# Kernel optimization log

Hardware: AMD Instinct MI355X
Metric: run time of the kernel (lower is better)

The kernel has to match this reference:

```python
import jax, jax.numpy as jnp
import numpy as np

EMB_DIM = 1024
ATT_DIM = 1024
N_HEADS = 16
HEAD_DIM = ATT_DIM // N_HEADS
ROPE_THETA = 10000.0


def setup_inputs() -> dict:
    key = jax.random.key(0)
    k1, k2, k3 = jax.random.split(key, 3)
    B, S = 2, 2048
    x = jax.random.normal(k1, (B, S, EMB_DIM), dtype=jnp.float32)
    # nn.Linear weights stored as [in, out] for x @ W
    W_qkv = jax.random.normal(k2, (EMB_DIM, 3 * ATT_DIM), dtype=jnp.float32) / np.sqrt(EMB_DIM)
    W_out = jax.random.normal(k3, (ATT_DIM, EMB_DIM), dtype=jnp.float32) / np.sqrt(ATT_DIM)
    return {"x": x, "W_qkv": W_qkv, "W_out": W_out}


def _rope_cos_sin(seq_len, dim, dtype):
    # rotary-embedding-torch: freqs over even indices, repeated interleaved
    inv_freq = 1.0 / (ROPE_THETA ** (jnp.arange(0, dim, 2, dtype=jnp.float32) / dim))
    t = jnp.arange(seq_len, dtype=jnp.float32)
    freqs = t[:, None] * inv_freq[None, :]            # [S, dim/2]
    freqs = jnp.repeat(freqs, 2, axis=-1)             # [S, dim] interleaved
    return jnp.cos(freqs).astype(dtype), jnp.sin(freqs).astype(dtype)


def _rotate_half(x):
    # interleaved pairs: (x0, x1) -> (-x1, x0)
    xr = x.reshape(x.shape[:-1] + (x.shape[-1] // 2, 2))
    x1, x2 = xr[..., 0], xr[..., 1]
    return jnp.stack([-x2, x1], axis=-1).reshape(x.shape)


def _apply_rope(x, cos, sin):
    # x: [B, H, S, D]; cos/sin: [S, D]
    return x * cos[None, None] + _rotate_half(x) * sin[None, None]


def reference(x, W_qkv, W_out):
    B, S, _ = x.shape
    qkv = x @ W_qkv                                   # [B, S, 3*ATT]
    qkv = qkv.reshape(B, S, 3, N_HEADS, HEAD_DIM)
    qkv = jnp.moveaxis(qkv, 3, 1)                     # [B, H, S, 3, D]
    q, k, v = qkv[..., 0, :], qkv[..., 1, :], qkv[..., 2, :]

    cos, sin = _rope_cos_sin(S, HEAD_DIM, x.dtype)
    q = _apply_rope(q, cos, sin)
    k = _apply_rope(k, cos, sin)

    scale = 1.0 / np.sqrt(HEAD_DIM)
    scores = jnp.einsum("bhqd,bhkd->bhqk", q, k) * scale
    attn = jax.nn.softmax(scores, axis=-1)
    out = jnp.einsum("bhqk,bhkd->bhqd", attn, v)      # [B, H, S, D]
    out = jnp.moveaxis(out, 1, 2).reshape(B, S, ATT_DIM)
    return out @ W_out                                # [B, S, EMB_DIM]
```

## Files before the change

kernel.cpp:

```cpp
#include <hip/hip_runtime.h>
#include <cstdint>
#include <cstddef>

typedef unsigned short u16;
typedef __bf16 bf16x8 __attribute__((ext_vector_type(8)));
typedef float f32x4 __attribute__((ext_vector_type(4)));

#define DEVI __device__ __forceinline__

constexpr int SEQ = 2048, NH = 16, HD = 64, EMB = 1024, N3 = 3072, MROWS = 4096;

DEVI u16 f2bf(float f) {
    union { float f; unsigned u; } x; x.f = f;
    unsigned r = (x.u + 0x7fffu + ((x.u >> 16) & 1u)) >> 16;
    return (u16)r;
}

DEVI f32x4 mfma16(bf16x8 a, bf16x8 b, f32x4 c) {
    return __builtin_amdgcn_mfma_f32_16x16x32_bf16(a, b, c, 0, 0, 0);
}

DEVI float exp2_raw(float x) {
    float r;
    asm("v_exp_f32 %0, %1" : "=v"(r) : "v"(x));
    return r;
}

#define GLDS16(g, l)                                                          \
    __builtin_amdgcn_global_load_lds(                                         \
        (__attribute__((address_space(1))) void*)(g),                         \
        (__attribute__((address_space(3))) void*)(l), 16, 0, 0)

__global__ __launch_bounds__(256) void prep_k(const float* __restrict__ x,
                                              const float* __restrict__ wqk,
                                              const float* __restrict__ wo,
                                              u16* __restrict__ xb, u16* __restrict__ wqkvT,
                                              u16* __restrict__ woutT, float2* __restrict__ tab) {
    __shared__ float tile[64][65];
    int bid = blockIdx.x, tid = threadIdx.x;
    if (bid < 4096) {
        int i = bid * 256 + tid;
        float4 v = ((const float4*)x)[i];
        ushort4 o;
        o.x = f2bf(v.x); o.y = f2bf(v.y); o.z = f2bf(v.z); o.w = f2bf(v.w);
        ((ushort4*)xb)[i] = o;
    } else if (bid < 5120) {
        const float* in; u16* out; int N, bx, by;
        if (bid < 4864) { in = wqk; out = wqkvT; N = 3072; int bb = bid - 4096; bx = bb % 48; by = bb / 48; }
        else            { in = wo;  out = woutT; N = 1024; int bb = bid - 4864; bx = bb % 16; by = bb / 16; }
        const int K = 1024;
        int k0 = by * 64, n0 = bx * 64;
        for (int i = 0; i < 16; i++) {
            int idx = i * 256 + tid;
            int r = idx >> 6, c = idx & 63;
            tile[r][c] = in[(size_t)(k0 + r) * N + n0 + c];
        }
        __syncthreads();
        for (int i = 0; i < 16; i++) {
            int idx = i * 256 + tid;
            int n = idx >> 6, k = idx & 63;
            out[(size_t)(n0 + n) * K + k0 + k] = f2bf(tile[k][n]);
        }
    } else {
        int idx = (bid - 5120) * 256 + tid;
        int t = idx >> 5, i = idx & 31;
        double ang = (double)t * pow(10000.0, -(double)i / 32.0);
        tab[idx] = make_float2((float)cos(ang), (float)sin(ang));
    }
}

template <int EPI>
__global__ __launch_bounds__(256) void gemm128_k(const u16* __restrict__ A, const u16* __restrict__ Bt,
                                                 int Kd, int Ncols,
                                                 u16* __restrict__ q_out, u16* __restrict__ k_out,
                                                 u16* __restrict__ v_out,
                                                 const float2* __restrict__ tab,
                                                 float* __restrict__ Cout) {
    __shared__ __align__(16) u16 smem[17408];
    u16* As = smem;
    u16* Bs = smem + 8192;
    int tid = threadIdx.x, lane = tid & 63, wv = tid >> 6;
    int wr = wv >> 1, wc = wv & 1;
    int l15 = lane & 15, lg = lane >> 4;
    int swr = l15 & 7;

    int nwg = gridDim.x * gridDim.y;
    int bid = blockIdx.y * gridDim.x + blockIdx.x;
    int swzb = (bid & 7) * (nwg >> 3) + (bid >> 3);
    int bx = swzb % gridDim.x, by = swzb / gridDim.x;
    int brow = by * 128, bcol = bx * 128;

    f32x4 acc[4][4];
    for (int i = 0; i < 4; i++)
        for (int j = 0; j < 4; j++) acc[i][j] = (f32x4){0.f, 0.f, 0.f, 0.f};

    const u16* Ab = A + (size_t)brow * Kd;
    const u16* Bb = Bt + (size_t)bcol * Kd;

    for (int kb = 0; kb < Kd; kb += 64) {
        for (int i = 0; i < 4; i++) {
            int cidx = i * 256 + tid;
            int rrow = cidx >> 3, c8 = cidx & 7;
            int sw = (c8 ^ (rrow & 7)) * 8;
            GLDS16(Ab + (size_t)rrow * Kd + kb + sw, As + cidx * 8);
            GLDS16(Bb + (size_t)rrow * Kd + kb + sw, Bs + cidx * 8);
        }
        __syncthreads();
#pragma unroll
        for (int kk = 0; kk < 2; kk++) {
            bf16x8 af[4], bf[4];
#pragma unroll
            for (int mi = 0; mi < 4; mi++)
                af[mi] = *(const bf16x8*)&As[(wr * 64 + mi * 16 + l15) * 64 +
                                             ((kk * 4 + lg) ^ swr) * 8];
#pragma unroll
            for (int ni = 0; ni < 4; ni++)
                bf[ni] = *(const bf16x8*)&Bs[(wc * 64 + ni * 16 + l15) * 64 +
                                             ((kk * 4 + lg) ^ swr) * 8];
#pragma unroll
            for (int mi = 0; mi < 4; mi++)
#pragma unroll
                for (int ni = 0; ni < 4; ni++)
                    acc[mi][ni] = mfma16(af[mi], bf[ni], acc[mi][ni]);
        }
        __syncthreads();
    }

    if constexpr (EPI == 0) {
        int c = bcol >> 10;
        int bb = brow >> 11, sbase = brow & 2047;
        int hbase = (bcol & 1023) >> 6;
        if (c == 2) {
            for (int mi = 0; mi < 4; mi++)
                for (int ni = 0; ni < 4; ni++) {
                    int col = wc * 64 + ni * 16 + l15;
                    int d = col & 63, h2 = col >> 6;
                    int s0 = sbase + wr * 64 + mi * 16 + lg * 4;
                    ushort4 pw;
                    pw.x = f2bf(acc[mi][ni][0]);
                    pw.y = f2bf(acc[mi][ni][1]);
                    pw.z = f2bf(acc[mi][ni][2]);
                    pw.w = f2bf(acc[mi][ni][3]);
                    *(ushort4*)&v_out[((size_t)(bb * NH + hbase + h2) * HD + d) * SEQ + s0] = pw;
                }
        } else {
            u16* dst = (c == 0) ? q_out : k_out;
            float sc = (c == 0) ? 0.125f * 1.4426950408889634f : 1.0f;
            u16* ep = smem;
            for (int mi = 0; mi < 4; mi++)
                for (int ni = 0; ni < 4; ni++) {
                    int col = wc * 64 + ni * 16 + l15;
                    int dg = col & 63;
                    for (int r = 0; r < 4; r++) {
                        int rowl = wr * 64 + mi * 16 + lg * 4 + r;
                        int s = sbase + rowl;
                        float val = acc[mi][ni][r];
                        float part = __shfl_xor(val, 1);
                        float2 cs = tab[(s << 5) | (dg >> 1)];
                        float o = (dg & 1) ? (val * cs.x + part * cs.y)
                                           : (val * cs.x - part * cs.y);
                        ep[rowl * 136 + (col ^ ((rowl & 7) << 3))] = f2bf(o * sc);
                    }
                }
            __syncthreads();
#pragma unroll
            for (int p = 0; p < 8; p++) {
                int unit = p * 32 + (tid >> 3);
                int h2 = unit >> 7, s_r = unit & 127, j = tid & 7;
                int cj = (h2 * 8 + j) ^ (s_r & 7);
                uint4 w = *(const uint4*)&ep[s_r * 136 + cj * 8];
                *(uint4*)&dst[(((size_t)(bb * NH + hbase + h2) * SEQ + sbase + s_r) << 6) +
                              j * 8] = w;
            }
        }
    } else {
        for (int mi = 0; mi < 4; mi++)
            for (int ni = 0; ni < 4; ni++) {
                int col = bcol + wc * 64 + ni * 16 + l15;
                for (int r = 0; r < 4; r++) {
                    int row = brow + wr * 64 + mi * 16 + lg * 4 + r;
                    Cout[(size_t)row * Ncols + col] = acc[mi][ni][r];
                }
            }
    }
}

__global__ __launch_bounds__(256, 2) void attn5_k(const u16* __restrict__ Qb,
                                                  const u16* __restrict__ Kb,
                                                  const u16* __restrict__ Vtg,
                                                  u16* __restrict__ Ob) {
    __shared__ __align__(16) u16 Ks[2][64 * 64];
    __shared__ __align__(16) u16 Vs[2][64 * 64];
    __shared__ __align__(16) u16 Pl[4][32 * 72];
    int tid = threadIdx.x, lane = tid & 63, wv = tid >> 6;
    int l15 = lane & 15, lg = lane >> 4;
    int swr = l15 & 7;
    int bh = blockIdx.y, b = bh >> 4, h = bh & 15;
    int qbase = blockIdx.x * 128;
    const size_t base = (size_t)bh * SEQ * HD;

    int c0 = tid, c1 = 256 + tid;
    int r0 = c0 >> 3, s0 = ((c0 & 7) ^ (r0 & 7)) * 8;
    int r1 = c1 >> 3, s1 = ((c1 & 7) ^ (r1 & 7)) * 8;
    const u16* kp0 = Kb + base + r0 * HD + s0;
    const u16* kp1 = Kb + base + r1 * HD + s1;
    const u16* vp0 = Vtg + base + (size_t)r0 * SEQ + s0;
    const u16* vp1 = Vtg + base + (size_t)r1 * SEQ + s1;

    bf16x8 qf[2][2];
#pragma unroll
    for (int u = 0; u < 2; u++)
#pragma unroll
        for (int kt = 0; kt < 2; kt++)
            qf[u][kt] = *(const bf16x8*)&Qb[base + (size_t)(qbase + wv * 32 + u * 16 + l15) * HD +
                                            kt * 32 + lg * 8];

    f32x4 oacc[2][4];
    float Lp[2] = {0.f, 0.f};
#pragma unroll
    for (int u = 0; u < 2; u++)
#pragma unroll
        for (int nt = 0; nt < 4; nt++) oacc[u][nt] = (f32x4){0.f, 0.f, 0.f, 0.f};

    auto stage = [&](int buf) {
        GLDS16(kp0, &Ks[buf][c0 * 8]);
        GLDS16(kp1, &Ks[buf][c1 * 8]);
        GLDS16(vp0, &Vs[buf][c0 * 8]);
        GLDS16(vp1, &Vs[buf][c1 * 8]);
        kp0 += 64 * HD; kp1 += 64 * HD;
        vp0 += 64; vp1 += 64;
    };

    stage(0);

    for (int it = 0; it < 32; ++it) {
        int buf = it & 1;
        __syncthreads();
        if (it < 31) stage(buf ^ 1);

        bf16x8 kf[4][2];
#pragma unroll
        for (int nt = 0; nt < 4; nt++)
#pragma unroll
            for (int kt = 0; kt < 2; kt++)
                kf[nt][kt] = *(const bf16x8*)&Ks[buf][(nt * 16 + l15) * 64 +
                                                     ((kt * 4 + lg) ^ swr) * 8];

#pragma unroll
        for (int u = 0; u < 2; u++) {
            f32x4 sa[4];
            __builtin_amdgcn_s_setprio(1);
#pragma unroll
            for (int nt = 0; nt < 4; nt++) {
                f32x4 z = (f32x4){0.f, 0.f, 0.f, 0.f};
#pragma unroll
                for (int kt = 0; kt < 2; kt++) z = mfma16(kf[nt][kt], qf[u][kt], z);
                sa[nt] = z;
            }
            __builtin_amdgcn_s_setprio(0);
            float ls = 0.f;
#pragma unroll
            for (int nt = 0; nt < 4; nt++) {
                float e0 = exp2_raw(sa[nt][0]), e1 = exp2_raw(sa[nt][1]);
                float e2 = exp2_raw(sa[nt][2]), e3 = exp2_raw(sa[nt][3]);
                ls += (e0 + e1) + (e2 + e3);
                unsigned p01, p23;
                asm("v_cvt_pk_bf16_f32 %0, %1, %2" : "=v"(p01) : "v"(e0), "v"(e1));
                asm("v_cvt_pk_bf16_f32 %0, %1, %2" : "=v"(p23) : "v"(e2), "v"(e3));
                uint2 pw; pw.x = p01; pw.y = p23;
                *(uint2*)&Pl[wv][(u * 16 + l15) * 72 + nt * 16 + lg * 4] = pw;
            }
            Lp[u] += ls;
        }

        bf16x8 pa[2][2];
#pragma unroll
        for (int u = 0; u < 2; u++)
#pragma unroll
            for (int kt = 0; kt < 2; kt++)
                pa[u][kt] = *(const bf16x8*)&Pl[wv][(u * 16 + l15) * 72 + kt * 32 + lg * 8];
        __builtin_amdgcn_s_setprio(1);
#pragma unroll
        for (int kt = 0; kt < 2; kt++)
#pragma unroll
            for (int nt = 0; nt < 4; nt++) {
                bf16x8 vf = *(const bf16x8*)&Vs[buf][(nt * 16 + l15) * 64 +
                                                    ((kt * 4 + lg) ^ swr) * 8];
#pragma unroll
                for (int u = 0; u < 2; u++) oacc[u][nt] = mfma16(pa[u][kt], vf, oacc[u][nt]);
            }
        __builtin_amdgcn_s_setprio(0);
    }

    float linv[2][4];
#pragma unroll
    for (int u = 0; u < 2; u++) {
        float L = Lp[u];
        L += __shfl_xor(L, 16);
        L += __shfl_xor(L, 32);
#pragma unroll
        for (int r = 0; r < 4; r++) linv[u][r] = 1.0f / __shfl(L, lg * 4 + r);
    }
#pragma unroll
    for (int u = 0; u < 2; u++)
#pragma unroll
        for (int nt = 0; nt < 4; nt++)
#pragma unroll
            for (int r = 0; r < 4; r++) {
                int row = qbase + wv * 32 + u * 16 + lg * 4 + r;
                Ob[(size_t)(b * SEQ + row) * EMB + h * HD + nt * 16 + l15] =
                    f2bf(oacc[u][nt][r] * linv[u][r]);
            }
}


extern "C" void kernel_launch(void* const* d_in, const int* in_sizes, int n_in,
                              void* d_out, int out_size, void* d_ws, size_t ws_size,
                              hipStream_t stream) {
    const float* x = (const float*)d_in[0];
    const float* wqk = (const float*)d_in[1];
    const float* wo = (const float*)d_in[2];
    float* out = (float*)d_out;
    char* ws = (char*)d_ws;

    u16* xb = (u16*)(ws + 0);
    u16* wqkvT = (u16*)(ws + 8388608);
    u16* woutT = (u16*)(ws + 14680064);
    u16* qb = (u16*)(ws + 16777216);
    u16* kb = (u16*)(ws + 25165824);
    u16* vb = (u16*)(ws + 33554432);
    u16* ao = (u16*)(ws + 41943040);
    float2* tab = (float2*)(ws + 50331648);

    prep_k<<<5376, 256, 0, stream>>>(x, wqk, wo, xb, wqkvT, woutT, tab);
    gemm128_k<0><<<dim3(N3 / 128, MROWS / 128), 256, 0, stream>>>(xb, wqkvT, EMB, N3, qb, kb, vb,
                                                                  tab, nullptr);
    attn5_k<<<dim3(SEQ / 128, 2 * NH), 256, 0, stream>>>(qb, kb, vb, ao);
    gemm128_k<1><<<dim3(EMB / 128, MROWS / 128), 256, 0, stream>>>(ao, woutT, EMB, EMB, nullptr,
                                                                   nullptr, nullptr, nullptr, out);
}
```

Measured before the change: 130.2 us.

## Double-buffer GEMM LDS tiles and raise attention occupancy hint

The 128x128 GEMM now keeps two LDS buffers for the A and B tiles and issues the next tile's global-to-LDS loads before computing on the current one. The goal is to hide global load latency behind the MFMA work, and it adds a barrier before the epilogue reuses shared memory. LDS per block doubles, which can lower GEMM occupancy. Separately, the attention kernel's launch bounds hint rises from 2 to 3 blocks per CU, which may force register spills.

```diff
diff --git a/kernel.cpp b/kernel.cpp
--- a/kernel.cpp
+++ b/kernel.cpp
@@ -76,9 +76,11 @@
                                                  u16* __restrict__ v_out,
                                                  const float2* __restrict__ tab,
                                                  float* __restrict__ Cout) {
-    __shared__ __align__(16) u16 smem[17408];
-    u16* As = smem;
-    u16* Bs = smem + 8192;
+    __shared__ __align__(16) u16 smem[32768];
+    u16* As0 = smem;
+    u16* As1 = smem + 8192;
+    u16* Bs0 = smem + 16384;
+    u16* Bs1 = smem + 24576;
     int tid = threadIdx.x, lane = tid & 63, wv = tid >> 6;
     int wr = wv >> 1, wc = wv & 1;
     int l15 = lane & 15, lg = lane >> 4;
@@ -94,28 +96,38 @@
     for (int i = 0; i < 4; i++)
         for (int j = 0; j < 4; j++) acc[i][j] = (f32x4){0.f, 0.f, 0.f, 0.f};
 
-    const u16* Ab = A + (size_t)brow * Kd;
-    const u16* Bb = Bt + (size_t)bcol * Kd;
-
-    for (int kb = 0; kb < Kd; kb += 64) {
+    const u16* aptr[4];
+    const u16* bptr[4];
+#pragma unroll
+    for (int i = 0; i < 4; i++) {
+        int cidx = i * 256 + tid;
+        int rrow = cidx >> 3, c8 = cidx & 7;
+        int sw = (c8 ^ (rrow & 7)) * 8;
+        aptr[i] = A + (size_t)(brow + rrow) * Kd + sw;
+        bptr[i] = Bt + (size_t)(bcol + rrow) * Kd + sw;
+    }
+
+    auto stageG = [&](u16* Ad, u16* Bd) {
+#pragma unroll
         for (int i = 0; i < 4; i++) {
-            int cidx = i * 256 + tid;
-            int rrow = cidx >> 3, c8 = cidx & 7;
-            int sw = (c8 ^ (rrow & 7)) * 8;
-            GLDS16(Ab + (size_t)rrow * Kd + kb + sw, As + cidx * 8);
-            GLDS16(Bb + (size_t)rrow * Kd + kb + sw, Bs + cidx * 8);
-        }
-        __syncthreads();
+            GLDS16(aptr[i], Ad + (i * 256 + tid) * 8);
+            GLDS16(bptr[i], Bd + (i * 256 + tid) * 8);
+            aptr[i] += 64;
+            bptr[i] += 64;
+        }
+    };
+
+    auto computeT = [&](const u16* Ar, const u16* Br) {
 #pragma unroll
         for (int kk = 0; kk < 2; kk++) {
             bf16x8 af[4], bf[4];
 #pragma unroll
             for (int mi = 0; mi < 4; mi++)
-                af[mi] = *(const bf16x8*)&As[(wr * 64 + mi * 16 + l15) * 64 +
+                af[mi] = *(const bf16x8*)&Ar[(wr * 64 + mi * 16 + l15) * 64 +
                                              ((kk * 4 + lg) ^ swr) * 8];
 #pragma unroll
             for (int ni = 0; ni < 4; ni++)
-                bf[ni] = *(const bf16x8*)&Bs[(wc * 64 + ni * 16 + l15) * 64 +
+                bf[ni] = *(const bf16x8*)&Br[(wc * 64 + ni * 16 + l15) * 64 +
                                              ((kk * 4 + lg) ^ swr) * 8];
 #pragma unroll
             for (int mi = 0; mi < 4; mi++)
@@ -123,7 +135,17 @@
                 for (int ni = 0; ni < 4; ni++)
                     acc[mi][ni] = mfma16(af[mi], bf[ni], acc[mi][ni]);
         }
+    };
+
+    int nIter = Kd >> 6;
+    stageG(As0, Bs0);
+    for (int it = 0; it < nIter; it += 2) {
         __syncthreads();
+        if (it + 1 < nIter) stageG(As1, Bs1);
+        computeT(As0, Bs0);
+        __syncthreads();
+        if (it + 2 < nIter) stageG(As0, Bs0);
+        computeT(As1, Bs1);
     }
 
     if constexpr (EPI == 0) {
@@ -147,6 +169,7 @@
             u16* dst = (c == 0) ? q_out : k_out;
             float sc = (c == 0) ? 0.125f * 1.4426950408889634f : 1.0f;
             u16* ep = smem;
+            __syncthreads();
             for (int mi = 0; mi < 4; mi++)
                 for (int ni = 0; ni < 4; ni++) {
                     int col = wc * 64 + ni * 16 + l15;
@@ -185,7 +208,7 @@
     }
 }
 
-__global__ __launch_bounds__(256, 2) void attn5_k(const u16* __restrict__ Qb,
+__global__ __launch_bounds__(256, 3) void attn5_k(const u16* __restrict__ Qb,
                                                   const u16* __restrict__ Kb,
                                                   const u16* __restrict__ Vtg,
                                                   u16* __restrict__ Ob) {
```

Measured after the change: 112.7 us. -13.4%, faster.
